# Kernel tuning notes

Hardware: AMD Instinct MI355X
Metric: run time of the kernel (lower is better)

The kernel has to match this reference:

```python
import jax, jax.numpy as jnp
import numpy as np

N = 8192      # num nodes
D = 128       # feature dim (input_dim)
E = 262144    # num edges (avg degree 32)
P = 4         # num perspectives (num_pers)
EPSILON = 0.3 # similarity threshold (args.epsilon)


def setup_inputs() -> dict:
    key = jax.random.key(0)
    k1, k2, k3, k4 = jax.random.split(key, 4)
    x = jax.random.normal(k1, (N, D), dtype=jnp.float32)
    ori_index = jax.random.randint(k2, (2, E), 0, N, dtype=jnp.int32)
    ori_weight = jax.random.uniform(k3, (E,), dtype=jnp.float32)
    w_pers = jax.random.normal(k4, (P, D), dtype=jnp.float32)  # weighted-cosine perspective weights
    return {"x": x, "ori_index": ori_index, "ori_weight": ori_weight, "w_pers": w_pers}


def reference(x, ori_index, ori_weight, w_pers):
    n = x.shape[0]
    # to_dense_adj: scatter edge weights into dense [N, N] adjacency (duplicate edges add)
    ori_g = jnp.zeros((n, n), dtype=x.dtype).at[ori_index[0], ori_index[1]].add(ori_weight)

    # GraphLearner (weighted multi-perspective cosine):
    # reweight features per perspective, L2-normalize, cosine sim, mean over perspectives
    xw = x[None, :, :] * w_pers[:, None, :]                              # [P, N, D]
    xn = xw / jnp.maximum(jnp.linalg.norm(xw, axis=-1, keepdims=True), 1e-12)
    sim = jnp.mean(jnp.einsum('pnd,pmd->pnm', xn, xn), axis=0)           # [N, N]
    # epsilon-thresholded learned graph
    sim_g = jnp.where(sim > EPSILON, sim, jnp.zeros_like(sim))

    # purified(sim, ori_g, epsilon): keep original edges where sim*ori_g > epsilon
    pur_g = jnp.where(sim * ori_g > EPSILON, ori_g, jnp.zeros_like(sim))
    new_g = pur_g + sim_g
    # dense_to_sparse has data-dependent output size; return the dense refined
    # adjacency (same information: edges = nonzero(new_g), weights = values).
    return new_g
```

## Files before the change

kernel.cpp:

```cpp
#include <hip/hip_runtime.h>
#include <hip/hip_bf16.h>
#include <stdint.h>

#define N_NODES 8192
#define DIM     128
#define KTOT    512
#define NEDGE   262144
#define EPS     0.3f
#define FIX_DELTA 0.0043f
#define FIX_CAP (1u << 19)
#define XCAP    (1u << 18)
#define LCAP    512
#define HASH_BITS 19
#define HASH_SLOTS (1u << HASH_BITS)

typedef unsigned int u32;
typedef unsigned short u16;
typedef __attribute__((ext_vector_type(8))) short short8;
typedef __attribute__((ext_vector_type(4))) float float4v;

#define OFF_YF  0u
#define OFF_YB  16777216u
#define OFF_CTR 25165824u
#define OFF_HK  25166080u
#define OFF_HV  27263232u
#define OFF_FL  29360384u
#define OFF_UL  31457536u
#define OFF_XL  32506112u
#define ZERO_VEC4 262160u

__device__ __forceinline__ u16 f2bf(float f) {
    u32 b = __builtin_bit_cast(u32, f);
    b += 0x7fffu + ((b >> 16) & 1u);
    return (u16)(b >> 16);
}

__global__ void prep_y(const float* __restrict__ x, const float* __restrict__ wp,
                       float* __restrict__ yf, u16* __restrict__ yb,
                       uint4* __restrict__ zbase) {
    if (blockIdx.x >= 2048) {
        for (u32 idx = (blockIdx.x - 2048) * 256 + threadIdx.x; idx < ZERO_VEC4;
             idx += 512 * 256)
            zbase[idx] = make_uint4(0, 0, 0, 0);
        return;
    }
    int node = blockIdx.x * 4 + (threadIdx.x >> 6);
    int lane = threadIdx.x & 63;
    float x0 = x[node * DIM + lane];
    float x1 = x[node * DIM + lane + 64];
    for (int p = 0; p < 4; ++p) {
        float v0 = x0 * wp[p * DIM + lane];
        float v1 = x1 * wp[p * DIM + lane + 64];
        float ss = v0 * v0 + v1 * v1;
        #pragma unroll
        for (int o = 1; o < 64; o <<= 1) ss += __shfl_xor(ss, o, 64);
        float scale = 0.5f / fmaxf(sqrtf(ss), 1e-12f);
        float y0 = v0 * scale, y1 = v1 * scale;
        int base = node * KTOT + p * DIM;
        yf[base + lane] = y0;       yf[base + lane + 64] = y1;
        yb[base + lane] = f2bf(y0); yb[base + lane + 64] = f2bf(y1);
    }
}

__global__ void edge_insert(const int* __restrict__ idx, const float* __restrict__ w,
                            u32* __restrict__ hkey, float* __restrict__ hval,
                            u32* __restrict__ ucnt, u32* __restrict__ ulist) {
    int e = blockIdx.x * 256 + threadIdx.x;
    u32 cell = (u32)(idx[e] * N_NODES + idx[NEDGE + e]);
    float wv = w[e];
    u32 key = cell + 1u;
    u32 h = (cell * 2654435761u) >> (32 - HASH_BITS);
    while (true) {
        u32 old = atomicCAS(&hkey[h], 0u, key);
        if (old == 0u) { ulist[atomicAdd(ucnt, 1u)] = h; atomicAdd(&hval[h], wv); break; }
        if (old == key) { atomicAdd(&hval[h], wv); break; }
        h = (h + 1u) & (HASH_SLOTS - 1u);
    }
}

#define TM  128
#define BK  64
#define TLD 132

__global__ __launch_bounds__(512)
void gemm_sim(const u16* __restrict__ yb, float* __restrict__ out,
              u32* __restrict__ fcnt, u32* __restrict__ flst) {
    int bm = blockIdx.y, bn = blockIdx.x;
    if (bm > bn) return;
    __shared__ __align__(16) char smem[64 * TLD * 4];
    u16* As = (u16*)smem;
    u16* Bs = As + TM * BK;
    float* tbuf = (float*)smem;
    __shared__ u32 s_cnt, s_base;
    __shared__ u32 s_list[LCAP];
    int tid = threadIdx.x;
    int lane = tid & 63, wid = tid >> 6;
    int wm = wid >> 1, wn = wid & 1;
    if (tid == 0) s_cnt = 0;

    float4v acc[2][4] = {};
    const u16* arow = yb + (size_t)(bm * TM) * KTOT;
    const u16* brow = yb + (size_t)(bn * TM) * KTOT;

    for (int kt = 0; kt < KTOT / BK; ++kt) {
        __syncthreads();
        #pragma unroll
        for (int q = 0; q < 2; ++q) {
            int c = q * 512 + wid * 64 + lane;
            int row = c >> 3;
            int kg = (c & 7) ^ (row & 7);
            __builtin_amdgcn_global_load_lds(
                (const __attribute__((address_space(1))) void*)(const void*)(arow + (size_t)row * KTOT + kt * BK + kg * 8),
                (__attribute__((address_space(3))) void*)(void*)(As + (q * 512 + wid * 64) * 8),
                16, 0, 0);
            __builtin_amdgcn_global_load_lds(
                (const __attribute__((address_space(1))) void*)(const void*)(brow + (size_t)row * KTOT + kt * BK + kg * 8),
                (__attribute__((address_space(3))) void*)(void*)(Bs + (q * 512 + wid * 64) * 8),
                16, 0, 0);
        }
        __syncthreads();
        #pragma unroll
        for (int kk = 0; kk < 2; ++kk) {
            short8 af[2], bfr[4];
            int kg2 = kk * 4 + (lane >> 4);
            int mrow = wm * 32 + (lane & 15);
            int ncol = wn * 64 + (lane & 15);
            #pragma unroll
            for (int i = 0; i < 2; ++i) {
                int ra = mrow + i * 16;
                af[i] = *(const short8*)&As[ra * BK + ((kg2 ^ (ra & 7)) * 8)];
            }
            #pragma unroll
            for (int j = 0; j < 4; ++j) {
                int rb = ncol + j * 16;
                bfr[j] = *(const short8*)&Bs[rb * BK + ((kg2 ^ (rb & 7)) * 8)];
            }
            #pragma unroll
            for (int i = 0; i < 2; ++i)
                #pragma unroll
                for (int j = 0; j < 4; ++j)
                    acc[i][j] = __builtin_amdgcn_mfma_f32_16x16x32_bf16(
                        af[i], bfr[j], acc[i][j], 0, 0, 0);
        }
    }

    int quad = lane >> 4, lcol = lane & 15;
    #pragma unroll
    for (int i = 0; i < 2; ++i)
        #pragma unroll
        for (int j = 0; j < 4; ++j) {
            int gr0 = bm * TM + wm * 32 + i * 16 + quad * 4;
            int gc  = bn * TM + wn * 64 + j * 16 + lcol;
            #pragma unroll
            for (int r = 0; r < 4; ++r) {
                float s = acc[i][j][r];
                __builtin_nontemporal_store(s > EPS ? s : 0.f,
                                            &out[(size_t)(gr0 + r) * N_NODES + gc]);
                if (fabsf(s - EPS) < FIX_DELTA) {
                    u32 cell = (u32)((gr0 + r) * N_NODES + gc);
                    u32 li = atomicAdd(&s_cnt, 1u);
                    if (li < LCAP) s_list[li] = cell;
                    else { u32 g = atomicAdd(fcnt, 1u); if (g < FIX_CAP) flst[g] = cell; }
                }
            }
        }

    #pragma unroll
    for (int h = 0; h < 2; ++h) {
        __syncthreads();
        if (wn == h) {
            #pragma unroll
            for (int i = 0; i < 2; ++i) {
                int Lr = wm * 32 + i * 16 + quad * 4;
                #pragma unroll
                for (int j = 0; j < 4; ++j) {
                    int Lc = j * 16 + lcol;
                    *(float4v*)&tbuf[Lc * TLD + Lr] = acc[i][j];
                }
            }
        }
        __syncthreads();
        #pragma unroll
        for (int v = 0; v < 4; ++v) {
            int chunk = v * 512 + tid;
            int row = chunk >> 5, c4 = chunk & 31;
            float4v t = *(const float4v*)&tbuf[row * TLD + c4 * 4];
            float4v o;
            #pragma unroll
            for (int r = 0; r < 4; ++r) o[r] = t[r] > EPS ? t[r] : 0.f;
            __builtin_nontemporal_store(o,
                (float4v*)&out[(size_t)(bn * TM + h * 64 + row) * N_NODES + bm * TM + c4 * 4]);
        }
    }

    __syncthreads();
    u32 cnt = s_cnt < LCAP ? s_cnt : LCAP;
    if (tid == 0) s_base = atomicAdd(fcnt, cnt);
    __syncthreads();
    for (u32 t = tid; t < cnt; t += 512) {
        u32 g = s_base + t;
        if (g < FIX_CAP) flst[g] = s_list[t];
    }
}

__device__ __forceinline__ float dot_exact(const float* __restrict__ yf,
                                           u32 i, u32 j, int tl) {
    const float4v* ri = (const float4v*)(yf + (size_t)i * KTOT);
    const float4v* rj = (const float4v*)(yf + (size_t)j * KTOT);
    float4v p = {};
    #pragma unroll
    for (int q = 0; q < 8; ++q) p += ri[q * 16 + tl] * rj[q * 16 + tl];
    float s = p.x + p.y + p.z + p.w;
    #pragma unroll
    for (int o = 8; o >= 1; o >>= 1) s += __shfl_xor(s, o, 16);
    return s;
}

__global__ void fix_and_edges(const float* __restrict__ yf,
                              const u32* __restrict__ fcnt, const u32* __restrict__ flst,
                              const u32* __restrict__ hkey, const float* __restrict__ hval,
                              const u32* __restrict__ ucnt, const u32* __restrict__ ulist,
                              float* __restrict__ out,
                              u32* __restrict__ xcnt, u32* __restrict__ xlist) {
    if (blockIdx.x < 1024) {
        u32 count = *fcnt; if (count > FIX_CAP) count = FIX_CAP;
        int team = (blockIdx.x * 256 + threadIdx.x) >> 4;
        int tl = threadIdx.x & 15;
        int nteams = 1024 * 16;
        for (u32 t = team; t < count; t += nteams) {
            u32 cell = flst[t];
            u32 i = cell >> 13, j = cell & 8191u;
            float s = dot_exact(yf, i, j, tl);
            if (tl == 0) {
                float v = s > EPS ? s : 0.f;
                out[(size_t)i * N_NODES + j] = v;
                out[(size_t)j * N_NODES + i] = v;
            }
        }
    } else {
        u32 count = *ucnt;
        for (u32 t = (blockIdx.x - 1024) * 256 + threadIdx.x; t < count; t += 512 * 256) {
            u32 h = ulist[t];
            u32 cell = hkey[h] - 1u;
            float a = hval[h];
            float sg = out[cell];
            bool hard = (a > 1.0f) ||
                        (fabsf(sg - EPS) < FIX_DELTA + 1e-6f) ||
                        (sg > 0.f && fabsf(sg * a - EPS) < FIX_DELTA * a + 1e-6f) ||
                        (sg == 0.f && a > 0.97f);
            if (hard) {
                u32 g = atomicAdd(xcnt, 1u);
                if (g < XCAP) xlist[g] = h;
            } else if (sg > 0.f) {
                out[cell] = sg + ((sg * a > EPS) ? a : 0.f);
            }
        }
    }
}

__global__ void edge_exact(const float* __restrict__ yf, const u32* __restrict__ hkey,
                           const float* __restrict__ hval, const u32* __restrict__ xcnt,
                           const u32* __restrict__ xlist, float* __restrict__ out) {
    u32 count = *xcnt; if (count > XCAP) count = XCAP;
    int team = (blockIdx.x * 256 + threadIdx.x) >> 4;
    int tl = threadIdx.x & 15;
    int nteams = gridDim.x * 16;
    for (u32 t = team; t < count; t += nteams) {
        u32 h = xlist[t];
        u32 cell = hkey[h] - 1u;
        float a = hval[h];
        u32 i = cell >> 13, j = cell & 8191u;
        float s = dot_exact(yf, i, j, tl);
        if (tl == 0) {
            float v = s > EPS ? s : 0.f;
            if (s * a > EPS) v += a;
            out[cell] = v;
        }
    }
}

extern "C" void kernel_launch(void* const* d_in, const int* in_sizes, int n_in,
                              void* d_out, int out_size, void* d_ws, size_t ws_size,
                              hipStream_t stream) {
    const float* x  = (const float*)d_in[0];
    const int*   oi = (const int*)d_in[1];
    const float* ow = (const float*)d_in[2];
    const float* wp = (const float*)d_in[3];
    float* out = (float*)d_out;
    char* ws = (char*)d_ws;
    float* yf = (float*)(ws + OFF_YF);
    u16*   yb = (u16*)(ws + OFF_YB);
    u32*   fc = (u32*)(ws + OFF_CTR);
    u32*   uc = (u32*)(ws + OFF_CTR + 4);
    u32*   xc = (u32*)(ws + OFF_CTR + 8);
    u32*   hk = (u32*)(ws + OFF_HK);
    float* hv = (float*)(ws + OFF_HV);
    u32*   fl = (u32*)(ws + OFF_FL);
    u32*   ul = (u32*)(ws + OFF_UL);
    u32*   xl = (u32*)(ws + OFF_XL);

    prep_y<<<2560, 256, 0, stream>>>(x, wp, yf, yb, (uint4*)(ws + OFF_CTR));
    edge_insert<<<NEDGE / 256, 256, 0, stream>>>(oi, ow, hk, hv, uc, ul);
    gemm_sim<<<dim3(N_NODES / TM, N_NODES / TM), 512, 0, stream>>>(yb, out, fc, fl);
    fix_and_edges<<<1536, 256, 0, stream>>>(yf, fc, fl, hk, hv, uc, ul, out, xc, xl);
    edge_exact<<<256, 256, 0, stream>>>(yf, hk, hv, xc, xl, out);
}
```

Before: 468.6 us.

## Compute full similarity grid instead of exploiting symmetry, with swizzled tile order

The GEMM kernel no longer computes only upper-triangle tiles and writes the transposed tile through shared memory. It now launches all 64x64 tiles and writes each tile once, using a 1D grid remapped into 8x8 groups for L2 locality on the shared operand rows. The fix-up pass now writes only the listed cell, since both (i,j) and (j,i) are enqueued separately. This removes the LDS transpose, its barriers and the strided transposed stores, at the cost of roughly doubling the MFMA work.

Measured after the change: 497.8 us. +6.2%, slower.

```diff
diff --git a/kernel.cpp b/kernel.cpp
--- a/kernel.cpp
+++ b/kernel.cpp
@@ -80,17 +80,16 @@
 
 #define TM  128
 #define BK  64
-#define TLD 132
 
 __global__ __launch_bounds__(512)
 void gemm_sim(const u16* __restrict__ yb, float* __restrict__ out,
               u32* __restrict__ fcnt, u32* __restrict__ flst) {
-    int bm = blockIdx.y, bn = blockIdx.x;
-    if (bm > bn) return;
-    __shared__ __align__(16) char smem[64 * TLD * 4];
-    u16* As = (u16*)smem;
-    u16* Bs = As + TM * BK;
-    float* tbuf = (float*)smem;
+    int o = blockIdx.x;
+    int g = o >> 3;
+    int bn = g >> 3;
+    int bm = (o & 7) + 8 * (g & 7);
+    __shared__ __align__(16) u16 As[TM * BK];
+    __shared__ __align__(16) u16 Bs[TM * BK];
     __shared__ u32 s_cnt, s_base;
     __shared__ u32 s_list[LCAP];
     int tid = threadIdx.x;
@@ -160,46 +159,17 @@
                     u32 cell = (u32)((gr0 + r) * N_NODES + gc);
                     u32 li = atomicAdd(&s_cnt, 1u);
                     if (li < LCAP) s_list[li] = cell;
-                    else { u32 g = atomicAdd(fcnt, 1u); if (g < FIX_CAP) flst[g] = cell; }
+                    else { u32 g2 = atomicAdd(fcnt, 1u); if (g2 < FIX_CAP) flst[g2] = cell; }
                 }
             }
         }
-
-    #pragma unroll
-    for (int h = 0; h < 2; ++h) {
-        __syncthreads();
-        if (wn == h) {
-            #pragma unroll
-            for (int i = 0; i < 2; ++i) {
-                int Lr = wm * 32 + i * 16 + quad * 4;
-                #pragma unroll
-                for (int j = 0; j < 4; ++j) {
-                    int Lc = j * 16 + lcol;
-                    *(float4v*)&tbuf[Lc * TLD + Lr] = acc[i][j];
-                }
-            }
-        }
-        __syncthreads();
-        #pragma unroll
-        for (int v = 0; v < 4; ++v) {
-            int chunk = v * 512 + tid;
-            int row = chunk >> 5, c4 = chunk & 31;
-            float4v t = *(const float4v*)&tbuf[row * TLD + c4 * 4];
-            float4v o;
-            #pragma unroll
-            for (int r = 0; r < 4; ++r) o[r] = t[r] > EPS ? t[r] : 0.f;
-            __builtin_nontemporal_store(o,
-                (float4v*)&out[(size_t)(bn * TM + h * 64 + row) * N_NODES + bm * TM + c4 * 4]);
-        }
-    }
-
     __syncthreads();
     u32 cnt = s_cnt < LCAP ? s_cnt : LCAP;
     if (tid == 0) s_base = atomicAdd(fcnt, cnt);
     __syncthreads();
     for (u32 t = tid; t < cnt; t += 512) {
-        u32 g = s_base + t;
-        if (g < FIX_CAP) flst[g] = s_list[t];
+        u32 g2 = s_base + t;
+        if (g2 < FIX_CAP) flst[g2] = s_list[t];
     }
 }
 
@@ -231,11 +201,7 @@
             u32 cell = flst[t];
             u32 i = cell >> 13, j = cell & 8191u;
             float s = dot_exact(yf, i, j, tl);
-            if (tl == 0) {
-                float v = s > EPS ? s : 0.f;
-                out[(size_t)i * N_NODES + j] = v;
-                out[(size_t)j * N_NODES + i] = v;
-            }
+            if (tl == 0) out[cell] = s > EPS ? s : 0.f;
         }
     } else {
         u32 count = *ucnt;
@@ -301,7 +267,7 @@
 
     prep_y<<<2560, 256, 0, stream>>>(x, wp, yf, yb, (uint4*)(ws + OFF_CTR));
     edge_insert<<<NEDGE / 256, 256, 0, stream>>>(oi, ow, hk, hv, uc, ul);
-    gemm_sim<<<dim3(N_NODES / TM, N_NODES / TM), 512, 0, stream>>>(yb, out, fc, fl);
+    gemm_sim<<<4096, 512, 0, stream>>>(yb, out, fc, fl);
     fix_and_edges<<<1536, 256, 0, stream>>>(yf, fc, fl, hk, hv, uc, ul, out, xc, xl);
     edge_exact<<<256, 256, 0, stream>>>(yf, hk, hv, xc, xl, out);
 }
```
